# Performance work log

Measured on AMD Instinct MI355X. Metric: run time of the kernel, lower is better.

## Reference

```python
import jax, jax.numpy as jnp
import numpy as np

B, T, I, H = 512, 512, 128, 256
EPS = 1e-5


def setup_inputs() -> dict:
    key = jax.random.key(0)
    ks = jax.random.split(key, 8)
    s_ih = 1.0 / np.sqrt(H)
    padded_X = jax.random.normal(ks[0], (B, T, I), dtype=jnp.float32)
    lengths = jax.random.randint(ks[1], (B,), 1, T + 1)  # in [1, T]
    # PyTorch LSTM params: W_ih (4H, I), W_hh (4H, H), biases (4H,), gate order [i,f,g,o]
    W_ih = jax.random.uniform(ks[2], (4 * H, I), minval=-s_ih, maxval=s_ih, dtype=jnp.float32)
    W_hh = jax.random.uniform(ks[3], (4 * H, H), minval=-s_ih, maxval=s_ih, dtype=jnp.float32)
    b_ih = jax.random.uniform(ks[4], (4 * H,), minval=-s_ih, maxval=s_ih, dtype=jnp.float32)
    b_hh = jax.random.uniform(ks[5], (4 * H,), minval=-s_ih, maxval=s_ih, dtype=jnp.float32)
    gamma = jnp.ones((H,), dtype=jnp.float32)
    beta = jnp.zeros((H,), dtype=jnp.float32)
    return {"padded_X": padded_X, "lengths": lengths, "W_ih": W_ih, "W_hh": W_hh,
            "b_ih": b_ih, "b_hh": b_hh, "gamma": gamma, "beta": beta}


def _lstm_last_hidden(padded_X, lengths, W_ih, W_hh, b_ih, b_hh):
    # Precompute input projections for all steps: (B, T, 4H)
    x_proj = jnp.einsum('bti,gi->btg', padded_X, W_ih) + b_ih + b_hh
    x_proj = jnp.swapaxes(x_proj, 0, 1)  # (T, B, 4H)
    ts = jnp.arange(padded_X.shape[1])

    def step(carry, inp):
        h, c = carry
        xp, t = inp
        gates = xp + h @ W_hh.T  # (B, 4H)
        i_g, f_g, g_g, o_g = jnp.split(gates, 4, axis=-1)
        i_g = jax.nn.sigmoid(i_g)
        f_g = jax.nn.sigmoid(f_g)
        g_g = jnp.tanh(g_g)
        o_g = jax.nn.sigmoid(o_g)
        c_new = f_g * c + i_g * g_g
        h_new = o_g * jnp.tanh(c_new)
        # freeze state once past the sequence length (packed-sequence semantics)
        valid = (t < lengths)[:, None]
        h = jnp.where(valid, h_new, h)
        c = jnp.where(valid, c_new, c)
        return (h, c), None

    h0 = jnp.zeros((padded_X.shape[0], W_hh.shape[1]), dtype=padded_X.dtype)
    c0 = jnp.zeros_like(h0)
    (h_fin, _), _ = jax.lax.scan(step, (h0, c0), (x_proj, ts))
    return h_fin  # (B, H) == h_n[-1]


def reference(padded_X, lengths, W_ih, W_hh, b_ih, b_hh, gamma, beta):
    h = _lstm_last_hidden(padded_X, lengths, W_ih, W_hh, b_ih, b_hh)
    mu = jnp.mean(h, axis=-1, keepdims=True)
    var = jnp.mean((h - mu) ** 2, axis=-1, keepdims=True)
    return (h - mu) / jnp.sqrt(var + EPS) * gamma + beta
```

## Files before the change

kernel.cpp:

```cpp
#include <hip/hip_runtime.h>

#define NB 512
#define NT 512
#define NI 128
#define NH 256
#define NG 1024
#define NMT 8
#define NWAVE 8
#define CH 4
#define EPSV 1e-5f

#define WXOFF 32768

typedef short short8 __attribute__((ext_vector_type(8)));
typedef float f32x4 __attribute__((ext_vector_type(4)));

__device__ __forceinline__ unsigned short f32_to_bf16(float f) {
  unsigned int u = __float_as_uint(f);
  u += 0x7fffu + ((u >> 16) & 1u);
  return (unsigned short)(u >> 16);
}
__device__ __forceinline__ float bf16_to_f32(unsigned short u) {
  return __uint_as_float(((unsigned int)u) << 16);
}

__global__ void prep_kernel(const float* __restrict__ W_ih, const float* __restrict__ W_hh,
                            const float* __restrict__ b_ih, const float* __restrict__ b_hh,
                            unsigned short* __restrict__ Wf, float* __restrict__ bsum) {
  int o = blockIdx.x * blockDim.x + threadIdx.x;
  int e = o & 7;
  int l = (o >> 3) & 63;
  int f = o >> 9;
  if (f < 512) {
    int kt = f & 7, m = (f >> 3) & 7, w = f >> 6;
    int row = w * 128 + m * 16 + (l & 15);
    int k = kt * 32 + ((l >> 4) << 3) + e;
    Wf[o] = f32_to_bf16(W_hh[row * NH + k]);
  } else if (f < 768) {
    int g = f - 512;
    int kx = g & 3, m = (g >> 2) & 7, w = g >> 5;
    int row = w * 128 + m * 16 + (l & 15);
    int k = kx * 32 + ((l >> 4) << 3) + e;
    Wf[o] = f32_to_bf16(W_ih[row * NI + k]);
  }
  if (o < NG) bsum[o] = b_ih[o] + b_hh[o];
}

__global__ void sort_kernel(const int* __restrict__ lengths, int* __restrict__ perm) {
  int i = threadIdx.x;
  __shared__ int L[NB];
  int li = lengths[i];
  L[i] = li;
  __syncthreads();
  int r = 0;
  for (int k = 0; k < NB; ++k) {
    int lk = L[k];
    r += (lk > li) || (lk == li && k < i);
  }
  perm[r] = i;
}

__global__ __launch_bounds__(512, 1)
void lstm_ln_kernel(const float* __restrict__ X, const int* __restrict__ lengths,
                    const int* __restrict__ perm,
                    const short8* __restrict__ Wf8, const float* __restrict__ bsum,
                    const float* __restrict__ gamma, const float* __restrict__ beta,
                    float* __restrict__ out) {
  const int p = blockIdx.x;
  const int tid = threadIdx.x;
  const int w = tid >> 6;
  const int l = tid & 63;

  __shared__ short8 ldsW[NWAVE * 16 * 64];
  __shared__ __align__(16) unsigned short gx[2 * CH][NG + 8];
  __shared__ __align__(16) float gh[2][NG];
  __shared__ __align__(16) unsigned short hbuf[2][NH];
  __shared__ float red[20];

  const int b0 = perm[2 * p];
  const int b1 = perm[2 * p + 1];
  const int len0 = lengths[b0];
  const int len1 = lengths[b1];
  const int lmax = (len0 > len1) ? len0 : len1;

  short8 wreg[NMT][4];
#pragma unroll
  for (int m = 0; m < NMT; ++m)
#pragma unroll
    for (int kt = 0; kt < 4; ++kt)
      wreg[m][kt] = Wf8[((w * 8 + m) * 8 + kt) * 64 + l];
#pragma unroll
  for (int m = 0; m < NMT; ++m) {
    ldsW[(w * 16 + m) * 64 + l]     = Wf8[((w * 8 + m) * 8 + 4) * 64 + l];
    ldsW[(w * 16 + 8 + m) * 64 + l] = Wf8[((w * 8 + m) * 8 + 5) * 64 + l];
  }

  const int s = tid >> 8;
  const int j = tid & 255;
  const int mylen = s ? len1 : len0;
  float c = 0.f, h = 0.f;

  const float* __restrict__ xr0 = X + (size_t)b0 * NT * NI;
  const float* __restrict__ xr1 = X + (size_t)b1 * NT * NI;
  const int seqb = l & 1;
  const int kg = l >> 4;
  const int st = (l >> 1) & 3;
  const float* __restrict__ xp = seqb ? xr1 : xr0;

  hbuf[s][j] = 0;
  __syncthreads();

  for (int t = 0; t < lmax; ++t) {
    if ((t & 3) == 0) {
      const float* xb = xp + (size_t)(t + st) * NI + kg * 8;
      const int cc = l & 15;
#pragma unroll
      for (int half = 0; half < 2; ++half) {
        f32x4 ax[4];
#pragma unroll
        for (int m = 0; m < 4; ++m) ax[m] = (f32x4){0.f, 0.f, 0.f, 0.f};
#pragma unroll
        for (int kx = 0; kx < 4; ++kx) {
          float4 xa = *(const float4*)(xb + kx * 32);
          float4 xc = *(const float4*)(xb + kx * 32 + 4);
          short8 bx;
          bx[0] = (short)f32_to_bf16(xa.x); bx[1] = (short)f32_to_bf16(xa.y);
          bx[2] = (short)f32_to_bf16(xa.z); bx[3] = (short)f32_to_bf16(xa.w);
          bx[4] = (short)f32_to_bf16(xc.x); bx[5] = (short)f32_to_bf16(xc.y);
          bx[6] = (short)f32_to_bf16(xc.z); bx[7] = (short)f32_to_bf16(xc.w);
#pragma unroll
          for (int m = 0; m < 4; ++m) {
            short8 wi = Wf8[WXOFF + ((w * 8 + half * 4 + m) * 4 + kx) * 64 + l];
            ax[m] = __builtin_amdgcn_mfma_f32_16x16x32_bf16(wi, bx, ax[m], 0, 0, 0);
          }
        }
        if (cc < 8) {
#pragma unroll
          for (int m = 0; m < 4; ++m) {
            int r0 = w * 128 + (half * 4 + m) * 16 + kg * 4;
            f32x4 bv = *(const f32x4*)&bsum[r0];
            ushort4 pk;
            pk.x = f32_to_bf16(ax[m][0] + bv[0]); pk.y = f32_to_bf16(ax[m][1] + bv[1]);
            pk.z = f32_to_bf16(ax[m][2] + bv[2]); pk.w = f32_to_bf16(ax[m][3] + bv[3]);
            *(ushort4*)&gx[cc][r0] = pk;
          }
        }
      }
    }

    f32x4 acc[NMT];
#pragma unroll
    for (int m = 0; m < NMT; ++m) acc[m] = (f32x4){0.f, 0.f, 0.f, 0.f};

    short8 swA[NMT];
#pragma unroll
    for (int m = 0; m < NMT; ++m) swA[m] = Wf8[((w * 8 + m) * 8 + 6) * 64 + l];

#pragma unroll
    for (int kt = 0; kt < 3; ++kt) {
      short8 bh = *(const short8*)&hbuf[seqb][kt * 32 + kg * 8];
#pragma unroll
      for (int m = 0; m < NMT; ++m)
        acc[m] = __builtin_amdgcn_mfma_f32_16x16x32_bf16(wreg[m][kt], bh, acc[m], 0, 0, 0);
    }
    {
      short8 bh = *(const short8*)&hbuf[seqb][6 * 32 + kg * 8];
#pragma unroll
      for (int m = 0; m < NMT; ++m)
        acc[m] = __builtin_amdgcn_mfma_f32_16x16x32_bf16(swA[m], bh, acc[m], 0, 0, 0);
    }
    short8 swB[NMT];
#pragma unroll
    for (int m = 0; m < NMT; ++m) swB[m] = Wf8[((w * 8 + m) * 8 + 7) * 64 + l];
    {
      short8 bh = *(const short8*)&hbuf[seqb][3 * 32 + kg * 8];
#pragma unroll
      for (int m = 0; m < NMT; ++m)
        acc[m] = __builtin_amdgcn_mfma_f32_16x16x32_bf16(wreg[m][3], bh, acc[m], 0, 0, 0);
    }
    {
      short8 bh = *(const short8*)&hbuf[seqb][4 * 32 + kg * 8];
#pragma unroll
      for (int m = 0; m < NMT; ++m)
        acc[m] = __builtin_amdgcn_mfma_f32_16x16x32_bf16(ldsW[(w * 16 + m) * 64 + l], bh,
                                                         acc[m], 0, 0, 0);
    }
    {
      short8 bh = *(const short8*)&hbuf[seqb][5 * 32 + kg * 8];
#pragma unroll
      for (int m = 0; m < NMT; ++m)
        acc[m] = __builtin_amdgcn_mfma_f32_16x16x32_bf16(ldsW[(w * 16 + 8 + m) * 64 + l], bh,
                                                         acc[m], 0, 0, 0);
    }
    {
      short8 bh = *(const short8*)&hbuf[seqb][7 * 32 + kg * 8];
#pragma unroll
      for (int m = 0; m < NMT; ++m)
        acc[m] = __builtin_amdgcn_mfma_f32_16x16x32_bf16(swB[m], bh, acc[m], 0, 0, 0);
    }

    if ((l & 15) < 2) {
#pragma unroll
      for (int m = 0; m < NMT; ++m)
        *(f32x4*)&gh[l & 1][w * 128 + m * 16 + kg * 4] = acc[m];
    }
    __syncthreads();

    {
      const int dt = ((t & 3) << 1) + s;
      float pi = gh[s][j]          + bf16_to_f32(gx[dt][j]);
      float pf = gh[s][NH + j]     + bf16_to_f32(gx[dt][NH + j]);
      float pg = gh[s][2 * NH + j] + bf16_to_f32(gx[dt][2 * NH + j]);
      float po = gh[s][3 * NH + j] + bf16_to_f32(gx[dt][3 * NH + j]);
      if (t < mylen) {
        float ig = 1.f / (1.f + __expf(-pi));
        float fg = 1.f / (1.f + __expf(-pf));
        float gv = 1.f - 2.f / (1.f + __expf(2.f * pg));
        float og = 1.f / (1.f + __expf(-po));
        c = fg * c + ig * gv;
        h = og * (1.f - 2.f / (1.f + __expf(2.f * c)));
        hbuf[s][j] = f32_to_bf16(h);
      }
    }
    __syncthreads();
  }

  float sum = h, sq = h * h;
#pragma unroll
  for (int off = 32; off > 0; off >>= 1) {
    sum += __shfl_xor(sum, off);
    sq  += __shfl_xor(sq, off);
  }
  if (l == 0) { red[w] = sum; red[8 + w] = sq; }
  __syncthreads();
  if (tid == 0) {
    float S = red[0] + red[1] + red[2] + red[3];
    float Q = red[8] + red[9] + red[10] + red[11];
    float mu = S * (1.f / NH);
    red[16] = mu;
    red[17] = rsqrtf(Q * (1.f / NH) - mu * mu + EPSV);
  }
  if (tid == 256) {
    float S = red[4] + red[5] + red[6] + red[7];
    float Q = red[12] + red[13] + red[14] + red[15];
    float mu = S * (1.f / NH);
    red[18] = mu;
    red[19] = rsqrtf(Q * (1.f / NH) - mu * mu + EPSV);
  }
  __syncthreads();
  {
    float mu = red[16 + 2 * s], rstd = red[17 + 2 * s];
    int b = s ? b1 : b0;
    out[(size_t)b * NH + j] = (h - mu) * rstd * gamma[j] + beta[j];
  }
}

extern "C" void kernel_launch(void* const* d_in, const int* in_sizes, int n_in,
                              void* d_out, int out_size, void* d_ws, size_t ws_size,
                              hipStream_t stream) {
  const float* X       = (const float*)d_in[0];
  const int*   lengths = (const int*)d_in[1];
  const float* W_ih    = (const float*)d_in[2];
  const float* W_hh    = (const float*)d_in[3];
  const float* b_ih    = (const float*)d_in[4];
  const float* b_hh    = (const float*)d_in[5];
  const float* gamma   = (const float*)d_in[6];
  const float* beta    = (const float*)d_in[7];
  float* out = (float*)d_out;

  unsigned short* Wf = (unsigned short*)d_ws;
  float* bsum = (float*)((char*)d_ws + (size_t)768 * 512 * sizeof(unsigned short));
  int* perm = (int*)((char*)bsum + NG * sizeof(float));

  int total = 768 * 512;
  prep_kernel<<<(total + 255) / 256, 256, 0, stream>>>(W_ih, W_hh, b_ih, b_hh, Wf, bsum);
  sort_kernel<<<1, NB, 0, stream>>>(lengths, perm);
  lstm_ln_kernel<<<NB / 2, 512, 0, stream>>>(X, lengths, perm, (const short8*)Wf, bsum,
                                             gamma, beta, out);
}
```

Measured before the change: 2.685 ms.

## Batch 16 sequences per block and fuse input projection into recurrent MFMA

```diff
diff --git a/kernel.cpp b/kernel.cpp
--- a/kernel.cpp
+++ b/kernel.cpp
@@ -7,7 +7,8 @@
 #define NG 1024
 #define NMT 8
 #define NWAVE 8
-#define CH 4
+#define SPB 16
+#define UPT 8
 #define EPSV 1e-5f
 
 #define WXOFF 32768
@@ -19,9 +20,6 @@
   unsigned int u = __float_as_uint(f);
   u += 0x7fffu + ((u >> 16) & 1u);
   return (unsigned short)(u >> 16);
-}
-__device__ __forceinline__ float bf16_to_f32(unsigned short u) {
-  return __uint_as_float(((unsigned int)u) << 16);
 }
 
 __global__ void prep_kernel(const float* __restrict__ W_ih, const float* __restrict__ W_hh,
@@ -71,187 +69,229 @@
   const int w = tid >> 6;
   const int l = tid & 63;
 
-  __shared__ short8 ldsW[NWAVE * 16 * 64];
-  __shared__ __align__(16) unsigned short gx[2 * CH][NG + 8];
-  __shared__ __align__(16) float gh[2][NG];
-  __shared__ __align__(16) unsigned short hbuf[2][NH];
-  __shared__ float red[20];
-
-  const int b0 = perm[2 * p];
-  const int b1 = perm[2 * p + 1];
-  const int len0 = lengths[b0];
-  const int len1 = lengths[b1];
-  const int lmax = (len0 > len1) ? len0 : len1;
-
-  short8 wreg[NMT][4];
+  __shared__ short8 ldsW[NWAVE * NMT * 64];
+  __shared__ __align__(16) f32x4 ghp[256 * 18];
+  __shared__ __align__(16) unsigned short hbuf[SPB][NH + 8];
+  __shared__ __align__(16) unsigned short xs[2][SPB][NI + 8];
+  __shared__ float redS[NWAVE][SPB];
+  __shared__ float redQ[NWAVE][SPB];
+  __shared__ float red2[2 * SPB];
+
+  short8 wreg[NMT][2];
 #pragma unroll
   for (int m = 0; m < NMT; ++m)
 #pragma unroll
-    for (int kt = 0; kt < 4; ++kt)
+    for (int kt = 0; kt < 2; ++kt)
       wreg[m][kt] = Wf8[((w * 8 + m) * 8 + kt) * 64 + l];
 #pragma unroll
-  for (int m = 0; m < NMT; ++m) {
-    ldsW[(w * 16 + m) * 64 + l]     = Wf8[((w * 8 + m) * 8 + 4) * 64 + l];
-    ldsW[(w * 16 + 8 + m) * 64 + l] = Wf8[((w * 8 + m) * 8 + 5) * 64 + l];
-  }
-
-  const int s = tid >> 8;
-  const int j = tid & 255;
-  const int mylen = s ? len1 : len0;
-  float c = 0.f, h = 0.f;
-
-  const float* __restrict__ xr0 = X + (size_t)b0 * NT * NI;
-  const float* __restrict__ xr1 = X + (size_t)b1 * NT * NI;
-  const int seqb = l & 1;
+  for (int m = 0; m < NMT; ++m)
+    ldsW[(w * 8 + m) * 64 + l] = Wf8[((w * 8 + m) * 8 + 2) * 64 + l];
+
+  const int s  = tid & 15;
+  const int jq = tid >> 4;
+  const int j0 = jq * UPT;
+  const int myb = perm[p * SPB + s];
+  const int mylen = lengths[myb];
+  const int lmax = lengths[perm[p * SPB]];
+  float c[UPT], h[UPT];
+#pragma unroll
+  for (int u = 0; u < UPT; ++u) { c[u] = 0.f; h[u] = 0.f; }
+
+  const int sx = tid >> 5;
+  const int xo = (tid & 31) * 4;
+  const float* __restrict__ xrow = X + (size_t)perm[p * SPB + sx] * NT * NI + xo;
+
+  for (int i = tid; i < SPB * (NH + 8); i += 512) (&hbuf[0][0])[i] = 0;
+
+  {
+    float4 xv = *(const float4*)(xrow);
+    ushort4 px;
+    px.x = f32_to_bf16(xv.x); px.y = f32_to_bf16(xv.y);
+    px.z = f32_to_bf16(xv.z); px.w = f32_to_bf16(xv.w);
+    *(ushort4*)&xs[0][sx][xo] = px;
+  }
+  float4 xnext = *(const float4*)(xrow + NI);
+  __syncthreads();
+
+  const int bn = l & 15;
   const int kg = l >> 4;
-  const int st = (l >> 1) & 3;
-  const float* __restrict__ xp = seqb ? xr1 : xr0;
-
-  hbuf[s][j] = 0;
-  __syncthreads();
 
   for (int t = 0; t < lmax; ++t) {
-    if ((t & 3) == 0) {
-      const float* xb = xp + (size_t)(t + st) * NI + kg * 8;
-      const int cc = l & 15;
-#pragma unroll
-      for (int half = 0; half < 2; ++half) {
-        f32x4 ax[4];
-#pragma unroll
-        for (int m = 0; m < 4; ++m) ax[m] = (f32x4){0.f, 0.f, 0.f, 0.f};
-#pragma unroll
-        for (int kx = 0; kx < 4; ++kx) {
-          float4 xa = *(const float4*)(xb + kx * 32);
-          float4 xc = *(const float4*)(xb + kx * 32 + 4);
-          short8 bx;
-          bx[0] = (short)f32_to_bf16(xa.x); bx[1] = (short)f32_to_bf16(xa.y);
-          bx[2] = (short)f32_to_bf16(xa.z); bx[3] = (short)f32_to_bf16(xa.w);
-          bx[4] = (short)f32_to_bf16(xc.x); bx[5] = (short)f32_to_bf16(xc.y);
-          bx[6] = (short)f32_to_bf16(xc.z); bx[7] = (short)f32_to_bf16(xc.w);
-#pragma unroll
-          for (int m = 0; m < 4; ++m) {
-            short8 wi = Wf8[WXOFF + ((w * 8 + half * 4 + m) * 4 + kx) * 64 + l];
-            ax[m] = __builtin_amdgcn_mfma_f32_16x16x32_bf16(wi, bx, ax[m], 0, 0, 0);
-          }
-        }
-        if (cc < 8) {
-#pragma unroll
-          for (int m = 0; m < 4; ++m) {
-            int r0 = w * 128 + (half * 4 + m) * 16 + kg * 4;
-            f32x4 bv = *(const f32x4*)&bsum[r0];
-            ushort4 pk;
-            pk.x = f32_to_bf16(ax[m][0] + bv[0]); pk.y = f32_to_bf16(ax[m][1] + bv[1]);
-            pk.z = f32_to_bf16(ax[m][2] + bv[2]); pk.w = f32_to_bf16(ax[m][3] + bv[3]);
-            *(ushort4*)&gx[cc][r0] = pk;
-          }
+    const int cur = t & 1;
+    f32x4 acc[NMT];
+#pragma unroll
+    for (int m = 0; m < NMT; ++m) acc[m] = (f32x4){0.f, 0.f, 0.f, 0.f};
+
+    short8 sA[NMT], sB[NMT];
+#pragma unroll
+    for (int m = 0; m < NMT; ++m) sA[m] = Wf8[WXOFF + ((w * 8 + m) * 4 + 0) * 64 + l];
+#pragma unroll
+    for (int m = 0; m < NMT; ++m) sB[m] = Wf8[WXOFF + ((w * 8 + m) * 4 + 1) * 64 + l];
+    {
+      short8 b = *(const short8*)&hbuf[bn][0 * 32 + kg * 8];
+#pragma unroll
+      for (int m = 0; m < NMT; ++m)
+        acc[m] = __builtin_amdgcn_mfma_f32_16x16x32_bf16(wreg[m][0], b, acc[m], 0, 0, 0);
+    }
+    {
+      short8 b = *(const short8*)&xs[cur][bn][0 * 32 + kg * 8];
+#pragma unroll
+      for (int m = 0; m < NMT; ++m)
+        acc[m] = __builtin_amdgcn_mfma_f32_16x16x32_bf16(sA[m], b, acc[m], 0, 0, 0);
+    }
+    short8 sC[NMT];
+#pragma unroll
+    for (int m = 0; m < NMT; ++m) sC[m] = Wf8[WXOFF + ((w * 8 + m) * 4 + 2) * 64 + l];
+    {
+      short8 b = *(const short8*)&hbuf[bn][1 * 32 + kg * 8];
+#pragma unroll
+      for (int m = 0; m < NMT; ++m)
+        acc[m] = __builtin_amdgcn_mfma_f32_16x16x32_bf16(wreg[m][1], b, acc[m], 0, 0, 0);
+    }
+    {
+      short8 b = *(const short8*)&xs[cur][bn][1 * 32 + kg * 8];
+#pragma unroll
+      for (int m = 0; m < NMT; ++m)
+        acc[m] = __builtin_amdgcn_mfma_f32_16x16x32_bf16(sB[m], b, acc[m], 0, 0, 0);
+    }
+    short8 sD[NMT];
+#pragma unroll
+    for (int m = 0; m < NMT; ++m) sD[m] = Wf8[WXOFF + ((w * 8 + m) * 4 + 3) * 64 + l];
+    {
+      short8 b = *(const short8*)&hbuf[bn][2 * 32 + kg * 8];
+#pragma unroll
+      for (int m = 0; m < NMT; ++m)
+        acc[m] = __builtin_amdgcn_mfma_f32_16x16x32_bf16(ldsW[(w * 8 + m) * 64 + l], b,
+                                                         acc[m], 0, 0, 0);
+    }
+    {
+      short8 b = *(const short8*)&xs[cur][bn][2 * 32 + kg * 8];
+#pragma unroll
+      for (int m = 0; m < NMT; ++m)
+        acc[m] = __builtin_amdgcn_mfma_f32_16x16x32_bf16(sC[m], b, acc[m], 0, 0, 0);
+    }
+    short8 sE[NMT];
+#pragma unroll
+    for (int m = 0; m < NMT; ++m) sE[m] = Wf8[((w * 8 + m) * 8 + 3) * 64 + l];
+    {
+      short8 b = *(const short8*)&xs[cur][bn][3 * 32 + kg * 8];
+#pragma unroll
+      for (int m = 0; m < NMT; ++m)
+        acc[m] = __builtin_amdgcn_mfma_f32_16x16x32_bf16(sD[m], b, acc[m], 0, 0, 0);
+    }
+    short8 sF[NMT];
+#pragma unroll
+    for (int m = 0; m < NMT; ++m) sF[m] = Wf8[((w * 8 + m) * 8 + 4) * 64 + l];
+    {
+      short8 b = *(const short8*)&hbuf[bn][3 * 32 + kg * 8];
+#pragma unroll
+      for (int m = 0; m < NMT; ++m)
+        acc[m] = __builtin_amdgcn_mfma_f32_16x16x32_bf16(sE[m], b, acc[m], 0, 0, 0);
+    }
+    short8 sG[NMT];
+#pragma unroll
+    for (int m = 0; m < NMT; ++m) sG[m] = Wf8[((w * 8 + m) * 8 + 5) * 64 + l];
+    {
+      short8 b = *(const short8*)&hbuf[bn][4 * 32 + kg * 8];
+#pragma unroll
+      for (int m = 0; m < NMT; ++m)
+        acc[m] = __builtin_amdgcn_mfma_f32_16x16x32_bf16(sF[m], b, acc[m], 0, 0, 0);
+    }
+    short8 sH[NMT];
+#pragma unroll
+    for (int m = 0; m < NMT; ++m) sH[m] = Wf8[((w * 8 + m) * 8 + 6) * 64 + l];
+    {
+      short8 b = *(const short8*)&hbuf[bn][5 * 32 + kg * 8];
+#pragma unroll
+      for (int m = 0; m < NMT; ++m)
+        acc[m] = __builtin_amdgcn_mfma_f32_16x16x32_bf16(sG[m], b, acc[m], 0, 0, 0);
+    }
+    short8 sI[NMT];
+#pragma unroll
+    for (int m = 0; m < NMT; ++m) sI[m] = Wf8[((w * 8 + m) * 8 + 7) * 64 + l];
+    {
+      short8 b = *(const short8*)&hbuf[bn][6 * 32 + kg * 8];
+#pragma unroll
+      for (int m = 0; m < NMT; ++m)
+        acc[m] = __builtin_amdgcn_mfma_f32_16x16x32_bf16(sH[m], b, acc[m], 0, 0, 0);
+    }
+    {
+      short8 b = *(const short8*)&hbuf[bn][7 * 32 + kg * 8];
+#pragma unroll
+      for (int m = 0; m < NMT; ++m)
+        acc[m] = __builtin_amdgcn_mfma_f32_16x16x32_bf16(sI[m], b, acc[m], 0, 0, 0);
+    }
+
+#pragma unroll
+    for (int m = 0; m < NMT; ++m) {
+      int rg = w * 128 + m * 16 + kg * 4;
+      f32x4 bv = *(const f32x4*)&bsum[rg];
+      ghp[(w * 32 + m * 4 + kg) * 18 + bn] = acc[m] + bv;
+    }
+    __syncthreads();
+
+    {
+      const bool live = (t < mylen);
+      float pi[UPT], pf[UPT], pg[UPT], po[UPT];
+#pragma unroll
+      for (int d = 0; d < 2; ++d) {
+        f32x4 qi = ghp[(0 * 64 + jq * 2 + d) * 18 + s];
+        f32x4 qf = ghp[(1 * 64 + jq * 2 + d) * 18 + s];
+        f32x4 qg = ghp[(2 * 64 + jq * 2 + d) * 18 + s];
+        f32x4 qo = ghp[(3 * 64 + jq * 2 + d) * 18 + s];
+#pragma unroll
+        for (int e = 0; e < 4; ++e) {
+          pi[d * 4 + e] = qi[e]; pf[d * 4 + e] = qf[e];
+          pg[d * 4 + e] = qg[e]; po[d * 4 + e] = qo[e];
         }
       }
-    }
-
-    f32x4 acc[NMT];
-#pragma unroll
-    for (int m = 0; m < NMT; ++m) acc[m] = (f32x4){0.f, 0.f, 0.f, 0.f};
-
-    short8 swA[NMT];
-#pragma unroll
-    for (int m = 0; m < NMT; ++m) swA[m] = Wf8[((w * 8 + m) * 8 + 6) * 64 + l];
-
-#pragma unroll
-    for (int kt = 0; kt < 3; ++kt) {
-      short8 bh = *(const short8*)&hbuf[seqb][kt * 32 + kg * 8];
-#pragma unroll
-      for (int m = 0; m < NMT; ++m)
-        acc[m] = __builtin_amdgcn_mfma_f32_16x16x32_bf16(wreg[m][kt], bh, acc[m], 0, 0, 0);
-    }
-    {
-      short8 bh = *(const short8*)&hbuf[seqb][6 * 32 + kg * 8];
-#pragma unroll
-      for (int m = 0; m < NMT; ++m)
-        acc[m] = __builtin_amdgcn_mfma_f32_16x16x32_bf16(swA[m], bh, acc[m], 0, 0, 0);
-    }
-    short8 swB[NMT];
-#pragma unroll
-    for (int m = 0; m < NMT; ++m) swB[m] = Wf8[((w * 8 + m) * 8 + 7) * 64 + l];
-    {
-      short8 bh = *(const short8*)&hbuf[seqb][3 * 32 + kg * 8];
-#pragma unroll
-      for (int m = 0; m < NMT; ++m)
-        acc[m] = __builtin_amdgcn_mfma_f32_16x16x32_bf16(wreg[m][3], bh, acc[m], 0, 0, 0);
-    }
-    {
-      short8 bh = *(const short8*)&hbuf[seqb][4 * 32 + kg * 8];
-#pragma unroll
-      for (int m = 0; m < NMT; ++m)
-        acc[m] = __builtin_amdgcn_mfma_f32_16x16x32_bf16(ldsW[(w * 16 + m) * 64 + l], bh,
-                                                         acc[m], 0, 0, 0);
-    }
-    {
-      short8 bh = *(const short8*)&hbuf[seqb][5 * 32 + kg * 8];
-#pragma unroll
-      for (int m = 0; m < NMT; ++m)
-        acc[m] = __builtin_amdgcn_mfma_f32_16x16x32_bf16(ldsW[(w * 16 + 8 + m) * 64 + l], bh,
-                                                         acc[m], 0, 0, 0);
-    }
-    {
-      short8 bh = *(const short8*)&hbuf[seqb][7 * 32 + kg * 8];
-#pragma unroll
-      for (int m = 0; m < NMT; ++m)
-        acc[m] = __builtin_amdgcn_mfma_f32_16x16x32_bf16(swB[m], bh, acc[m], 0, 0, 0);
-    }
-
-    if ((l & 15) < 2) {
-#pragma unroll
-      for (int m = 0; m < NMT; ++m)
-        *(f32x4*)&gh[l & 1][w * 128 + m * 16 + kg * 4] = acc[m];
+      if (live) {
+        short8 hb;
+#pragma unroll
+        for (int u = 0; u < UPT; ++u) {
+          float ig = 1.f / (1.f + __expf(-pi[u]));
+          float fg = 1.f / (1.f + __expf(-pf[u]));
+          float gv = 1.f - 2.f / (1.f + __expf(2.f * pg[u]));
+          float og = 1.f / (1.f + __expf(-po[u]));
+          c[u] = fg * c[u] + ig * gv;
+          h[u] = og * (1.f - 2.f / (1.f + __expf(2.f * c[u])));
+          hb[u] = (short)f32_to_bf16(h[u]);
+        }
+        *(short8*)&hbuf[s][j0] = hb;
+      }
+      ushort4 px;
+      px.x = f32_to_bf16(xnext.x); px.y = f32_to_bf16(xnext.y);
+      px.z = f32_to_bf16(xnext.z); px.w = f32_to_bf16(xnext.w);
+      *(ushort4*)&xs[(t + 1) & 1][sx][xo] = px;
+      int tn = (t + 2 < NT) ? (t + 2) : (NT - 1);
+      xnext = *(const float4*)(xrow + (size_t)tn * NI);
     }
     __syncthreads();
-
-    {
-      const int dt = ((t & 3) << 1) + s;
-      float pi = gh[s][j]          + bf16_to_f32(gx[dt][j]);
-      float pf = gh[s][NH + j]     + bf16_to_f32(gx[dt][NH + j]);
-      float pg = gh[s][2 * NH + j] + bf16_to_f32(gx[dt][2 * NH + j]);
-      float po = gh[s][3 * NH + j] + bf16_to_f32(gx[dt][3 * NH + j]);
-      if (t < mylen) {
-        float ig = 1.f / (1.f + __expf(-pi));
-        float fg = 1.f / (1.f + __expf(-pf));
-        float gv = 1.f - 2.f / (1.f + __expf(2.f * pg));
-        float og = 1.f / (1.f + __expf(-po));
-        c = fg * c + ig * gv;
-        h = og * (1.f - 2.f / (1.f + __expf(2.f * c)));
-        hbuf[s][j] = f32_to_bf16(h);
-      }
-    }
-    __syncthreads();
-  }
-
-  float sum = h, sq = h * h;
-#pragma unroll
-  for (int off = 32; off > 0; off >>= 1) {
-    sum += __shfl_xor(sum, off);
-    sq  += __shfl_xor(sq, off);
-  }
-  if (l == 0) { red[w] = sum; red[8 + w] = sq; }
+  }
+
+  float S = 0.f, Q = 0.f;
+#pragma unroll
+  for (int u = 0; u < UPT; ++u) { S += h[u]; Q += h[u] * h[u]; }
+  S += __shfl_xor(S, 16); Q += __shfl_xor(Q, 16);
+  S += __shfl_xor(S, 32); Q += __shfl_xor(Q, 32);
+  if (l < SPB) { redS[w][l] = S; redQ[w][l] = Q; }
   __syncthreads();
-  if (tid == 0) {
-    float S = red[0] + red[1] + red[2] + red[3];
-    float Q = red[8] + red[9] + red[10] + red[11];
-    float mu = S * (1.f / NH);
-    red[16] = mu;
-    red[17] = rsqrtf(Q * (1.f / NH) - mu * mu + EPSV);
-  }
-  if (tid == 256) {
-    float S = red[4] + red[5] + red[6] + red[7];
-    float Q = red[12] + red[13] + red[14] + red[15];
-    float mu = S * (1.f / NH);
-    red[18] = mu;
-    red[19] = rsqrtf(Q * (1.f / NH) - mu * mu + EPSV);
+  if (tid < SPB) {
+    float Sa = 0.f, Qa = 0.f;
+#pragma unroll
+    for (int ww = 0; ww < NWAVE; ++ww) { Sa += redS[ww][tid]; Qa += redQ[ww][tid]; }
+    float mu = Sa * (1.f / NH);
+    red2[tid] = mu;
+    red2[SPB + tid] = rsqrtf(Qa * (1.f / NH) - mu * mu + EPSV);
   }
   __syncthreads();
   {
-    float mu = red[16 + 2 * s], rstd = red[17 + 2 * s];
-    int b = s ? b1 : b0;
-    out[(size_t)b * NH + j] = (h - mu) * rstd * gamma[j] + beta[j];
+    float mu = red2[s], rstd = red2[SPB + s];
+#pragma unroll
+    for (int u = 0; u < UPT; ++u) {
+      int j = j0 + u;
+      out[(size_t)myb * NH + j] = (h[u] - mu) * rstd * gamma[j] + beta[j];
+    }
   }
 }
 
@@ -275,6 +315,6 @@
   int total = 768 * 512;
   prep_kernel<<<(total + 255) / 256, 256, 0, stream>>>(W_ih, W_hh, b_ih, b_hh, Wf, bsum);
   sort_kernel<<<1, NB, 0, stream>>>(lengths, perm);
-  lstm_ln_kernel<<<NB / 2, 512, 0, stream>>>(X, lengths, perm, (const short8*)Wf, bsum,
-                                             gamma, beta, out);
-}
+  lstm_ln_kernel<<<NB / SPB, 512, 0, stream>>>(X, lengths, perm, (const short8*)Wf, bsum,
+                                               gamma, beta, out);
+}
```

Result: slower. 7.622 ms (+183.9%).
